# Kernel tuning notes

Hardware: AMD Instinct MI355X
Metric: run time of the kernel (lower is better)

The kernel has to match this reference:

```python
import jax, jax.numpy as jnp
import numpy as np

TEMPERATURE = 0.5
EPS = 1e-12  # F.normalize eps


def setup_inputs() -> dict:
    key = jax.random.key(0)
    z = jax.random.normal(key, (2048, 8, 256), dtype=jnp.float32)
    return {"z": z}


def reference(z):
    B, D = z.shape[0], z.shape[1]
    z = z.reshape(B, D, -1)  # [B, D, F]
    # F.normalize along features
    norm = jnp.linalg.norm(z, axis=-1, keepdims=True)
    zn = z / jnp.maximum(norm, EPS)

    # Positive term: per sample b, sim among D views -> [B, D, D], off-diagonal sum
    sim_pos = jnp.exp(jnp.einsum('bdf,bef->bde', zn, zn) / TEMPERATURE)
    eye_d = jnp.eye(D, dtype=bool)
    pos = jnp.sum(jnp.where(eye_d[None], 0.0, sim_pos), axis=(1, 2))  # [B]

    # Negative term: per view d, sim among B samples -> [D, B, B], row-wise off-diag mean, summed over views
    sim_neg = jnp.exp(jnp.einsum('bdf,cdf->dbc', zn, zn) / TEMPERATURE)
    eye_b = jnp.eye(B, dtype=bool)
    neg = jnp.sum(jnp.where(eye_b[None], 0.0, sim_neg), axis=-1) / (B - 1)  # [D, B]
    neg = jnp.sum(neg, axis=0)  # [B]

    logits = pos / (pos + neg)  # [B]
    # torch CrossEntropyLoss(reduction='sum') with 1-D input [C] and float target ones(C):
    # loss = -sum_c target_c * log_softmax(logits)_c = -sum(log_softmax(logits))
    error = -jnp.sum(jax.nn.log_softmax(logits))
    return error / B
```

## Files before the change

### kernel.cpp

```cpp
#include <hip/hip_runtime.h>
#include <hip/hip_bf16.h>

#define B_N 2048
#define D_V 8
#define F_D 256

typedef __attribute__((ext_vector_type(8))) short short8;
typedef __attribute__((ext_vector_type(4))) float floatx4;

__device__ inline unsigned short f2bf(float f) {
    __hip_bfloat16 h = __float2bfloat16(f);
    return *reinterpret_cast<unsigned short*>(&h);
}

__device__ inline float wave_reduce_sum(float v) {
    #pragma unroll
    for (int off = 1; off < 64; off <<= 1)
        v += __shfl_xor(v, off, 64);
    return v;
}

__global__ void norm_kernel(const float* __restrict__ z,
                            unsigned short* __restrict__ zn) {
    int wave = (blockIdx.x * blockDim.x + threadIdx.x) >> 6;
    int lane = threadIdx.x & 63;
    const float4* zp = (const float4*)(z + (size_t)wave * F_D);
    float4 v = zp[lane];
    float ss = v.x * v.x + v.y * v.y + v.z * v.z + v.w * v.w;
    ss = wave_reduce_sum(ss);
    float inv = 1.0f / fmaxf(sqrtf(ss), 1e-12f);
    int b = wave >> 3, d = wave & 7;
    unsigned short* op = zn + (size_t)d * (B_N * F_D) + (size_t)b * F_D + lane * 4;
    ushort4 o;
    o.x = f2bf(v.x * inv);
    o.y = f2bf(v.y * inv);
    o.z = f2bf(v.z * inv);
    o.w = f2bf(v.w * inv);
    *(ushort4*)op = o;
}

__global__ void pos_kernel(const unsigned short* __restrict__ zn,
                           float* __restrict__ pos) {
    int gw = (blockIdx.x * blockDim.x + threadIdx.x) >> 6;
    int lane = threadIdx.x & 63;
    int q = lane >> 4, li = lane & 15;
    int s0 = gw * 2;
    int b = s0 + (li >> 3), d = li & 7;
    const unsigned short* rowp = zn + (size_t)d * (B_N * F_D) + (size_t)b * F_D;
    short8 a[8];
    #pragma unroll
    for (int kk = 0; kk < 8; kk++)
        a[kk] = *(const short8*)(rowp + kk * 32 + q * 8);
    floatx4 acc = {0.f, 0.f, 0.f, 0.f};
    #pragma unroll
    for (int kk = 0; kk < 8; kk++)
        acc = __builtin_amdgcn_mfma_f32_16x16x32_bf16(a[kk], a[kk], acc, 0, 0, 0);
    float p0 = 0.f, p1 = 0.f;
    #pragma unroll
    for (int r = 0; r < 4; r++) {
        int row = q * 4 + r, col = li;
        bool same_sample = (row >> 3) == (col >> 3);
        if (same_sample && row != col) {
            float e = __expf(2.0f * acc[r]);
            if (row < 8) p0 += e; else p1 += e;
        }
    }
    p0 = wave_reduce_sum(p0);
    p1 = wave_reduce_sum(p1);
    if (lane == 0) { pos[s0] = p0; pos[s0 + 1] = p1; }
}

#define BCOLS 64
#define LSTRIDE 264

__global__ void neg_kernel(const unsigned short* __restrict__ zn,
                           float* __restrict__ negsum) {
    __shared__ __align__(16) unsigned short Bs[BCOLS * LSTRIDE];
    const int d = blockIdx.z;
    const unsigned short* Z = zn + (size_t)d * (B_N * F_D);
    int tid = threadIdx.x;
    int w = tid >> 6, lane = tid & 63;
    int q = lane >> 4, li = lane & 15;
    int r0 = blockIdx.x * 128 + w * 32;
    int c_base = blockIdx.y * 512;

    short8 a0[8], a1[8];
    #pragma unroll
    for (int kk = 0; kk < 8; kk++) {
        a0[kk] = *(const short8*)(Z + (size_t)(r0 + li) * F_D + kk * 32 + q * 8);
        a1[kk] = *(const short8*)(Z + (size_t)(r0 + 16 + li) * F_D + kk * 32 + q * 8);
    }
    float rs0[4] = {0.f, 0.f, 0.f, 0.f}, rs1[4] = {0.f, 0.f, 0.f, 0.f};

    for (int stage = 0; stage < 512 / BCOLS; ++stage) {
        int c0 = c_base + stage * BCOLS;
        __syncthreads();
        #pragma unroll
        for (int it = 0; it < 8; ++it) {
            int idx = it * 256 + tid;
            int row = idx >> 5;
            int kc = idx & 31;
            *(short8*)(&Bs[row * LSTRIDE + kc * 8]) =
                *(const short8*)(Z + (size_t)(c0 + row) * F_D + kc * 8);
        }
        __syncthreads();
        #pragma unroll
        for (int ct = 0; ct < BCOLS / 16; ++ct) {
            short8 bf[8];
            #pragma unroll
            for (int kk = 0; kk < 8; kk++)
                bf[kk] = *(const short8*)(&Bs[(ct * 16 + li) * LSTRIDE + kk * 32 + q * 8]);
            floatx4 acc0 = {0.f, 0.f, 0.f, 0.f}, acc1 = {0.f, 0.f, 0.f, 0.f};
            #pragma unroll
            for (int kk = 0; kk < 8; kk++) {
                acc0 = __builtin_amdgcn_mfma_f32_16x16x32_bf16(a0[kk], bf[kk], acc0, 0, 0, 0);
                acc1 = __builtin_amdgcn_mfma_f32_16x16x32_bf16(a1[kk], bf[kk], acc1, 0, 0, 0);
            }
            int gc0 = c0 + ct * 16;
            bool diag0 = (gc0 == r0);
            bool diag1 = (gc0 == r0 + 16);
            #pragma unroll
            for (int r = 0; r < 4; ++r) {
                float e0 = __expf(2.0f * acc0[r]);
                float e1 = __expf(2.0f * acc1[r]);
                int rloc = q * 4 + r;
                if (!(diag0 && li == rloc)) rs0[r] += e0;
                if (!(diag1 && li == rloc)) rs1[r] += e1;
            }
        }
    }
    #pragma unroll
    for (int off = 1; off < 16; off <<= 1) {
        #pragma unroll
        for (int r = 0; r < 4; r++) {
            rs0[r] += __shfl_xor(rs0[r], off, 64);
            rs1[r] += __shfl_xor(rs1[r], off, 64);
        }
    }
    if (li == 0) {
        #pragma unroll
        for (int r = 0; r < 4; r++) {
            atomicAdd(&negsum[r0 + q * 4 + r], rs0[r]);
            atomicAdd(&negsum[r0 + 16 + q * 4 + r], rs1[r]);
        }
    }
}

__global__ void final_kernel(const float* __restrict__ pos,
                             const float* __restrict__ negsum,
                             float* __restrict__ out) {
    __shared__ float red[256];
    int t = threadIdx.x;
    float vals[8];
    float lmax = -1e30f;
    #pragma unroll
    for (int i = 0; i < 8; i++) {
        int idx = t * 8 + i;
        float p = pos[idx];
        float n = negsum[idx] * (1.0f / (float)(B_N - 1));
        float l = p / (p + n);
        vals[i] = l;
        lmax = fmaxf(lmax, l);
    }
    red[t] = lmax; __syncthreads();
    for (int s = 128; s > 0; s >>= 1) {
        if (t < s) red[t] = fmaxf(red[t], red[t + s]);
        __syncthreads();
    }
    float m = red[0]; __syncthreads();
    float se = 0.f, sl = 0.f;
    #pragma unroll
    for (int i = 0; i < 8; i++) { se += expf(vals[i] - m); sl += vals[i]; }
    red[t] = se; __syncthreads();
    for (int s = 128; s > 0; s >>= 1) {
        if (t < s) red[t] += red[t + s];
        __syncthreads();
    }
    float S = red[0]; __syncthreads();
    red[t] = sl; __syncthreads();
    for (int s = 128; s > 0; s >>= 1) {
        if (t < s) red[t] += red[t + s];
        __syncthreads();
    }
    if (t == 0) out[0] = m + logf(S) - red[0] / (float)B_N;
}

extern "C" void kernel_launch(void* const* d_in, const int* in_sizes, int n_in,
                              void* d_out, int out_size, void* d_ws, size_t ws_size,
                              hipStream_t stream) {
    const float* z = (const float*)d_in[0];
    float* out = (float*)d_out;
    unsigned short* zn = (unsigned short*)d_ws;
    float* negsum = (float*)((char*)d_ws + (size_t)D_V * B_N * F_D * 2);
    float* pos = negsum + B_N;

    hipMemsetAsync(negsum, 0, B_N * sizeof(float), stream);
    norm_kernel<<<dim3(4096), 256, 0, stream>>>(z, zn);
    pos_kernel<<<dim3(256), 256, 0, stream>>>(zn, pos);
    neg_kernel<<<dim3(16, 4, 8), 256, 0, stream>>>(zn, negsum);
    final_kernel<<<1, 256, 0, stream>>>(pos, negsum, out);
}
```

Measured before the change: 106.8 us.

## Exploit Gram symmetry in neg kernel with upper-triangular tiles and column sums

```diff
diff --git a/kernel.cpp b/kernel.cpp
--- a/kernel.cpp
+++ b/kernel.cpp
@@ -4,6 +4,9 @@
 #define B_N 2048
 #define D_V 8
 #define F_D 256
+#define TILE 128
+#define BC 64
+#define LSTR 264
 
 typedef __attribute__((ext_vector_type(8))) short short8;
 typedef __attribute__((ext_vector_type(4))) float floatx4;
@@ -21,8 +24,11 @@
 }
 
 __global__ void norm_kernel(const float* __restrict__ z,
-                            unsigned short* __restrict__ zn) {
-    int wave = (blockIdx.x * blockDim.x + threadIdx.x) >> 6;
+                            unsigned short* __restrict__ zn,
+                            float* __restrict__ ns8) {
+    int gid = blockIdx.x * blockDim.x + threadIdx.x;
+    if (gid < D_V * B_N) ns8[gid] = 0.0f;
+    int wave = gid >> 6;
     int lane = threadIdx.x & 63;
     const float4* zp = (const float4*)(z + (size_t)wave * F_D);
     float4 v = zp[lane];
@@ -70,84 +76,106 @@
     if (lane == 0) { pos[s0] = p0; pos[s0 + 1] = p1; }
 }
 
-#define BCOLS 64
-#define LSTRIDE 264
-
-__global__ void neg_kernel(const unsigned short* __restrict__ zn,
-                           float* __restrict__ negsum) {
-    __shared__ __align__(16) unsigned short Bs[BCOLS * LSTRIDE];
-    const int d = blockIdx.z;
+__global__ __launch_bounds__(128, 2)
+void neg_kernel(const unsigned short* __restrict__ zn,
+                float* __restrict__ ns8) {
+    __shared__ __align__(16) unsigned short Bs[BC * LSTR];
+    __shared__ float csred[2][TILE];
+    const int d = blockIdx.y;
+    int trem = blockIdx.x;
+    int i = 0;
+    while (trem >= 16 - i) { trem -= 16 - i; ++i; }
+    const int j = i + trem;
+    const bool diag = (i == j);
     const unsigned short* Z = zn + (size_t)d * (B_N * F_D);
-    int tid = threadIdx.x;
-    int w = tid >> 6, lane = tid & 63;
+    int tid = threadIdx.x, w = tid >> 6, lane = tid & 63;
     int q = lane >> 4, li = lane & 15;
-    int r0 = blockIdx.x * 128 + w * 32;
-    int c_base = blockIdx.y * 512;
-
-    short8 a0[8], a1[8];
-    #pragma unroll
-    for (int kk = 0; kk < 8; kk++) {
-        a0[kk] = *(const short8*)(Z + (size_t)(r0 + li) * F_D + kk * 32 + q * 8);
-        a1[kk] = *(const short8*)(Z + (size_t)(r0 + 16 + li) * F_D + kk * 32 + q * 8);
-    }
-    float rs0[4] = {0.f, 0.f, 0.f, 0.f}, rs1[4] = {0.f, 0.f, 0.f, 0.f};
-
-    for (int stage = 0; stage < 512 / BCOLS; ++stage) {
-        int c0 = c_base + stage * BCOLS;
-        __syncthreads();
-        #pragma unroll
-        for (int it = 0; it < 8; ++it) {
-            int idx = it * 256 + tid;
-            int row = idx >> 5;
-            int kc = idx & 31;
-            *(short8*)(&Bs[row * LSTRIDE + kc * 8]) =
+    int r0 = i * TILE + w * 64;
+
+    short8 a[4][8];
+    #pragma unroll
+    for (int s = 0; s < 4; s++)
+        #pragma unroll
+        for (int kk = 0; kk < 8; kk++)
+            a[s][kk] = *(const short8*)(Z + (size_t)(r0 + s * 16 + li) * F_D + kk * 32 + q * 8);
+
+    float rs[4][4];
+    #pragma unroll
+    for (int s = 0; s < 4; s++)
+        #pragma unroll
+        for (int r = 0; r < 4; r++) rs[s][r] = 0.f;
+    float cacc[2] = {0.f, 0.f};
+
+    for (int stage = 0; stage < 2; ++stage) {
+        int c0 = j * TILE + stage * BC;
+        __syncthreads();
+        #pragma unroll
+        for (int it = 0; it < 16; ++it) {
+            int idx = it * 128 + tid;
+            int row = idx >> 5, kc = idx & 31;
+            *(short8*)(&Bs[row * LSTR + kc * 8]) =
                 *(const short8*)(Z + (size_t)(c0 + row) * F_D + kc * 8);
         }
         __syncthreads();
         #pragma unroll
-        for (int ct = 0; ct < BCOLS / 16; ++ct) {
+        for (int ct = 0; ct < 4; ++ct) {
             short8 bf[8];
             #pragma unroll
             for (int kk = 0; kk < 8; kk++)
-                bf[kk] = *(const short8*)(&Bs[(ct * 16 + li) * LSTRIDE + kk * 32 + q * 8]);
-            floatx4 acc0 = {0.f, 0.f, 0.f, 0.f}, acc1 = {0.f, 0.f, 0.f, 0.f};
-            #pragma unroll
-            for (int kk = 0; kk < 8; kk++) {
-                acc0 = __builtin_amdgcn_mfma_f32_16x16x32_bf16(a0[kk], bf[kk], acc0, 0, 0, 0);
-                acc1 = __builtin_amdgcn_mfma_f32_16x16x32_bf16(a1[kk], bf[kk], acc1, 0, 0, 0);
+                bf[kk] = *(const short8*)(&Bs[(ct * 16 + li) * LSTR + kk * 32 + q * 8]);
+            floatx4 acc[4];
+            #pragma unroll
+            for (int s = 0; s < 4; s++) acc[s] = (floatx4){0.f, 0.f, 0.f, 0.f};
+            #pragma unroll
+            for (int kk = 0; kk < 8; kk++)
+                #pragma unroll
+                for (int s = 0; s < 4; s++)
+                    acc[s] = __builtin_amdgcn_mfma_f32_16x16x32_bf16(a[s][kk], bf[kk], acc[s], 0, 0, 0);
+            int gcol = c0 + ct * 16 + li;
+            float csum = 0.f;
+            #pragma unroll
+            for (int s = 0; s < 4; s++) {
+                #pragma unroll
+                for (int r = 0; r < 4; r++) {
+                    float e = __expf(2.0f * acc[s][r]);
+                    int grow = r0 + s * 16 + q * 4 + r;
+                    e = (diag && grow == gcol) ? 0.f : e;
+                    rs[s][r] += e;
+                    csum += e;
+                }
             }
-            int gc0 = c0 + ct * 16;
-            bool diag0 = (gc0 == r0);
-            bool diag1 = (gc0 == r0 + 16);
-            #pragma unroll
-            for (int r = 0; r < 4; ++r) {
-                float e0 = __expf(2.0f * acc0[r]);
-                float e1 = __expf(2.0f * acc1[r]);
-                int rloc = q * 4 + r;
-                if (!(diag0 && li == rloc)) rs0[r] += e0;
-                if (!(diag1 && li == rloc)) rs1[r] += e1;
-            }
+            csum += __shfl_xor(csum, 16, 64);
+            csum += __shfl_xor(csum, 32, 64);
+            if (q == ct) cacc[stage] += csum;
         }
     }
-    #pragma unroll
-    for (int off = 1; off < 16; off <<= 1) {
-        #pragma unroll
-        for (int r = 0; r < 4; r++) {
-            rs0[r] += __shfl_xor(rs0[r], off, 64);
-            rs1[r] += __shfl_xor(rs1[r], off, 64);
-        }
-    }
+
+    #pragma unroll
+    for (int off = 1; off < 16; off <<= 1)
+        #pragma unroll
+        for (int s = 0; s < 4; s++)
+            #pragma unroll
+            for (int r = 0; r < 4; r++)
+                rs[s][r] += __shfl_xor(rs[s][r], off, 64);
     if (li == 0) {
         #pragma unroll
-        for (int r = 0; r < 4; r++) {
-            atomicAdd(&negsum[r0 + q * 4 + r], rs0[r]);
-            atomicAdd(&negsum[r0 + 16 + q * 4 + r], rs1[r]);
-        }
+        for (int s = 0; s < 4; s++)
+            #pragma unroll
+            for (int r = 0; r < 4; r++)
+                atomicAdd(&ns8[d * B_N + r0 + s * 16 + q * 4 + r], rs[s][r]);
+    }
+
+    csred[w][lane] = cacc[0];
+    csred[w][64 + lane] = cacc[1];
+    __syncthreads();
+    if (!diag && tid < TILE) {
+        float v = csred[0][tid] + csred[1][tid];
+        atomicAdd(&ns8[d * B_N + j * TILE + tid], v);
     }
 }
 
 __global__ void final_kernel(const float* __restrict__ pos,
-                             const float* __restrict__ negsum,
+                             const float* __restrict__ ns8,
                              float* __restrict__ out) {
     __shared__ float red[256];
     int t = threadIdx.x;
@@ -156,8 +184,11 @@
     #pragma unroll
     for (int i = 0; i < 8; i++) {
         int idx = t * 8 + i;
+        float nsum = 0.f;
+        #pragma unroll
+        for (int d = 0; d < D_V; d++) nsum += ns8[d * B_N + idx];
         float p = pos[idx];
-        float n = negsum[idx] * (1.0f / (float)(B_N - 1));
+        float n = nsum * (1.0f / (float)(B_N - 1));
         float l = p / (p + n);
         vals[i] = l;
         lmax = fmaxf(lmax, l);
@@ -191,12 +222,11 @@
     const float* z = (const float*)d_in[0];
     float* out = (float*)d_out;
     unsigned short* zn = (unsigned short*)d_ws;
-    float* negsum = (float*)((char*)d_ws + (size_t)D_V * B_N * F_D * 2);
-    float* pos = negsum + B_N;
-
-    hipMemsetAsync(negsum, 0, B_N * sizeof(float), stream);
-    norm_kernel<<<dim3(4096), 256, 0, stream>>>(z, zn);
+    float* ns8 = (float*)((char*)d_ws + (size_t)D_V * B_N * F_D * 2);
+    float* pos = ns8 + D_V * B_N;
+
+    norm_kernel<<<dim3(4096), 256, 0, stream>>>(z, zn, ns8);
     pos_kernel<<<dim3(256), 256, 0, stream>>>(zn, pos);
-    neg_kernel<<<dim3(16, 4, 8), 256, 0, stream>>>(zn, negsum);
-    final_kernel<<<1, 256, 0, stream>>>(pos, negsum, out);
-}
+    neg_kernel<<<dim3(136, 8), 128, 0, stream>>>(zn, ns8);
+    final_kernel<<<1, 256, 0, stream>>>(pos, ns8, out);
+}
```

Result: faster. 96.22 us (median of 2 runs) (-9.9%).
